# Optimization experiments

Measured on AMD Instinct MI355X. Metric: run time of the kernel, lower is better.

## Reference

```python
import jax, jax.numpy as jnp
import numpy as np

T, B, I, H = 512, 64, 512, 512

def setup_inputs() -> dict:
    key = jax.random.key(0)
    ks = jax.random.split(key, 7)
    s_in = 1.0 / np.sqrt(H)
    return {
        "input": jax.random.normal(ks[0], (T, B, I), dtype=jnp.float32),
        "h0": jax.random.normal(ks[1], (B, H), dtype=jnp.float32),
        "c0": jax.random.normal(ks[2], (B, H), dtype=jnp.float32),
        "W_ih": jax.random.uniform(ks[3], (4 * H, I), dtype=jnp.float32, minval=-s_in, maxval=s_in),
        "W_hh": jax.random.uniform(ks[4], (4 * H, H), dtype=jnp.float32, minval=-s_in, maxval=s_in),
        "b_ih": jax.random.uniform(ks[5], (4 * H,), dtype=jnp.float32, minval=-s_in, maxval=s_in),
        "b_hh": jax.random.uniform(ks[6], (4 * H,), dtype=jnp.float32, minval=-s_in, maxval=s_in),
    }

def reference(input, h0, c0, W_ih, W_hh, b_ih, b_hh):
    # Precompute input projections for all timesteps: [T, B, 4H]
    x_proj = jnp.einsum('tbi,gi->tbg', input, W_ih) + b_ih + b_hh

    def step(state, xp):
        h, c = state
        gates = xp + h @ W_hh.T  # [B, 4H]
        i_g, f_g, g_g, o_g = jnp.split(gates, 4, axis=-1)
        i_g = jax.nn.sigmoid(i_g)
        f_g = jax.nn.sigmoid(f_g)
        g_g = jnp.tanh(g_g)
        o_g = jax.nn.sigmoid(o_g)
        c_new = f_g * c + i_g * g_g
        h_new = o_g * jnp.tanh(c_new)
        return (h_new, c_new), h_new

    # reverse=True: process last timestep first, outputs placed at original indices
    (h_f, c_f), outputs = jax.lax.scan(step, (h0, c0), x_proj, reverse=True)
    return outputs, h_f, c_f
```

## Files before the change

### kernel.cpp

```cpp
#include <hip/hip_runtime.h>
#include <math.h>
#include <stdint.h>

#define T_ 512
#define B_ 64
#define I_ 512
#define H_ 512
#define G_ 2048
#define K_ 1024
#define NMR 32
#define NCOL 4
#define NBLK (NMR * NCOL)

typedef __bf16 bf16x8 __attribute__((ext_vector_type(8)));
typedef float f32x4 __attribute__((ext_vector_type(4)));
typedef int i32x4 __attribute__((ext_vector_type(4)));

#define OFF_W    ((size_t)0)
#define OFF_BIAS (OFF_W + (size_t)G_ * K_ * 2)
#define OFF_HSWZ (OFF_BIAS + (size_t)G_ * 4)
#define OFF_BAR  (OFF_HSWZ + (size_t)2 * H_ * B_ * 2)
#define OFF_XSWZ (OFF_BAR + 1024)


__global__ void prep_w(const float* __restrict__ W_ih, const float* __restrict__ W_hh,
                       const float* __restrict__ b_ih, const float* __restrict__ b_hh,
                       char* __restrict__ ws) {
    __bf16* W = (__bf16*)(ws + OFF_W);
    float* bias = (float*)(ws + OFF_BIAS);
    int idx = blockIdx.x * 256 + threadIdx.x;
    int g = idx >> 10;
    int k = idx & (K_ - 1);
    float v = (k < I_) ? W_ih[g * I_ + k] : W_hh[g * H_ + (k - I_)];
    W[idx] = (__bf16)v;
    if (idx < G_) bias[idx] = b_ih[idx] + b_hh[idx];
    if (idx < 256) ((unsigned*)(ws + OFF_BAR))[idx] = 0u;
}

__global__ void prep_x(const float* __restrict__ input, char* __restrict__ ws) {
    __bf16* xswz = (__bf16*)(ws + OFF_XSWZ);
    int s = blockIdx.x * 256 + threadIdx.x;
    int lane = s & 63;
    int nblk = (s >> 6) & 3;
    int kblk = (s >> 8) & 15;
    int t = s >> 12;
    int b = nblk * 16 + (lane & 15);
    int k = kblk * 32 + (lane >> 4) * 8;
    const float* src = input + ((size_t)t * B_ + b) * I_ + k;
    float4 v0 = *(const float4*)src;
    float4 v1 = *(const float4*)(src + 4);
    bf16x8 o;
    o[0]=(__bf16)v0.x; o[1]=(__bf16)v0.y; o[2]=(__bf16)v0.z; o[3]=(__bf16)v0.w;
    o[4]=(__bf16)v1.x; o[5]=(__bf16)v1.y; o[6]=(__bf16)v1.z; o[7]=(__bf16)v1.w;
    *(bf16x8*)(xswz + (size_t)s * 8) = o;
}

__global__ void prep_h0(const float* __restrict__ h0, char* __restrict__ ws) {
    __bf16* hswz0 = (__bf16*)(ws + OFF_HSWZ);
    int s = blockIdx.x * 256 + threadIdx.x;
    int lane = s & 63;
    int nblk = (s >> 6) & 3;
    int hk = s >> 8;
    int b = nblk * 16 + (lane & 15);
    int u = hk * 32 + (lane >> 4) * 8;
    const float* src = h0 + (size_t)b * H_ + u;
    float4 v0 = *(const float4*)src;
    float4 v1 = *(const float4*)(src + 4);
    bf16x8 o;
    o[0]=(__bf16)v0.x; o[1]=(__bf16)v0.y; o[2]=(__bf16)v0.z; o[3]=(__bf16)v0.w;
    o[4]=(__bf16)v1.x; o[5]=(__bf16)v1.y; o[6]=(__bf16)v1.z; o[7]=(__bf16)v1.w;
    *(bf16x8*)(hswz0 + (size_t)s * 8) = o;
}

__device__ __forceinline__ float sigmoid_f(float x) { return 1.f / (1.f + __expf(-x)); }
__device__ __forceinline__ float tanh_f(float x) { return 1.f - 2.f / (1.f + __expf(2.f * x)); }

__launch_bounds__(256, 1)
__global__ void lstm_persist(const float* __restrict__ c0, float* out,
                             char* __restrict__ ws) {
    __shared__ __bf16 xbuf[8192];
    __shared__ __bf16 hbuf[8192];
    __shared__ float gl[4][16][17];
    __shared__ __bf16 hstage[2][16][8];

    const __bf16* W = (const __bf16*)(ws + OFF_W);
    const float* bias = (const float*)(ws + OFF_BIAS);
    __bf16* Hswz = (__bf16*)(ws + OFF_HSWZ);
    const __bf16* Xswz = (const __bf16*)(ws + OFF_XSWZ);
    unsigned* flags = (unsigned*)(ws + OFF_BAR);

    const int tid = threadIdx.x;
    const int wave = tid >> 6;
    const int lane = tid & 63;
    const int l16 = lane & 15;
    const int quad = lane >> 4;
    const int wgM = blockIdx.x & 31;
    const int wgN = blockIdx.x >> 5;

    bf16x8 A[32];
    {
        const size_t arow = (size_t)(wave * H_ + wgM * 16 + l16) * K_ + quad * 8;
        #pragma unroll
        for (int ks = 0; ks < 32; ++ks)
            A[ks] = *(const bf16x8*)(W + arow + ks * 32);
    }

    const int cu_u = tid & 15;
    const int cu_bl = tid >> 4;
    const int hu = wgM * 16 + cu_u;
    const int batch = wgN * 16 + cu_bl;
    float creg = c0[(size_t)batch * H_ + hu];
    const float bias_i = bias[hu];
    const float bias_f = bias[H_ + hu];
    const float bias_g = bias[2 * H_ + hu];
    const float bias_o = bias[3 * H_ + hu];

    #define ISSUE_X(tt) do {                                                          \
        const __bf16* xb_ = Xswz + (size_t)(tt) * 32768;                              \
        _Pragma("unroll")                                                             \
        for (int i_ = 0; i_ < 4; ++i_) {                                              \
            const int kb_ = wave * 4 + i_;                                            \
            __builtin_amdgcn_global_load_lds(                                         \
                (const __attribute__((address_space(1))) void*)(xb_ + (size_t)((kb_ * 4 + wgN) * 64 + lane) * 8), \
                (__attribute__((address_space(3))) void*)(xbuf + kb_ * 512),          \
                16, 0, 0);                                                            \
        }                                                                             \
    } while (0)

    ISSUE_X(T_ - 1);
    asm volatile("s_waitcnt vmcnt(0)" ::: "memory");
    __builtin_amdgcn_sched_barrier(0);

    for (int t = T_ - 1; ; --t) {
        if (t < T_ - 1 && wave == 1) {
            const unsigned target = (unsigned)(T_ - 1 - t);
            const unsigned long long faddr =
                (unsigned long long)(uintptr_t)(flags + wgN * 64 + (lane & 31));
            unsigned cur;
            do {
                asm volatile("global_load_dword %0, %1, off sc0 sc1\n\t"
                             "s_waitcnt vmcnt(0)"
                             : "=v"(cur) : "v"(faddr) : "memory");
            } while (!__all(lane >= 32 || lane == wgM || cur >= target));
        }
        __builtin_amdgcn_sched_barrier(0);
        __builtin_amdgcn_s_barrier();
        __builtin_amdgcn_sched_barrier(0);

        {
            const __bf16* hb = Hswz + (size_t)((t + 1) & 1) * 32768;
            #pragma unroll
            for (int i = 0; i < 4; ++i) {
                const int hk = wave * 4 + i;
                __builtin_amdgcn_global_load_lds(
                    (const __attribute__((address_space(1))) void*)(hb + (size_t)((hk * 4 + wgN) * 64 + lane) * 8),
                    (__attribute__((address_space(3))) void*)(hbuf + hk * 512),
                    16, 0, 0x11);
            }
        }

        f32x4 ac0 = {0,0,0,0}, ac1 = {0,0,0,0}, ac2 = {0,0,0,0}, ac3 = {0,0,0,0};
        #pragma unroll
        for (int f = 0; f < 4; ++f) {
            bf16x8 b0 = *(const bf16x8*)(xbuf + (4*f+0) * 512 + lane * 8);
            bf16x8 b1 = *(const bf16x8*)(xbuf + (4*f+1) * 512 + lane * 8);
            bf16x8 b2 = *(const bf16x8*)(xbuf + (4*f+2) * 512 + lane * 8);
            bf16x8 b3 = *(const bf16x8*)(xbuf + (4*f+3) * 512 + lane * 8);
            ac0 = __builtin_amdgcn_mfma_f32_16x16x32_bf16(A[4*f+0], b0, ac0, 0, 0, 0);
            ac1 = __builtin_amdgcn_mfma_f32_16x16x32_bf16(A[4*f+1], b1, ac1, 0, 0, 0);
            ac2 = __builtin_amdgcn_mfma_f32_16x16x32_bf16(A[4*f+2], b2, ac2, 0, 0, 0);
            ac3 = __builtin_amdgcn_mfma_f32_16x16x32_bf16(A[4*f+3], b3, ac3, 0, 0, 0);
        }

        asm volatile("s_waitcnt vmcnt(0)" ::: "memory");
        __builtin_amdgcn_sched_barrier(0);
        __builtin_amdgcn_s_barrier();
        __builtin_amdgcn_sched_barrier(0);

        #pragma unroll
        for (int f = 0; f < 4; ++f) {
            bf16x8 b0 = *(const bf16x8*)(hbuf + (4*f+0) * 512 + lane * 8);
            bf16x8 b1 = *(const bf16x8*)(hbuf + (4*f+1) * 512 + lane * 8);
            bf16x8 b2 = *(const bf16x8*)(hbuf + (4*f+2) * 512 + lane * 8);
            bf16x8 b3 = *(const bf16x8*)(hbuf + (4*f+3) * 512 + lane * 8);
            ac0 = __builtin_amdgcn_mfma_f32_16x16x32_bf16(A[16+4*f+0], b0, ac0, 0, 0, 0);
            ac1 = __builtin_amdgcn_mfma_f32_16x16x32_bf16(A[16+4*f+1], b1, ac1, 0, 0, 0);
            ac2 = __builtin_amdgcn_mfma_f32_16x16x32_bf16(A[16+4*f+2], b2, ac2, 0, 0, 0);
            ac3 = __builtin_amdgcn_mfma_f32_16x16x32_bf16(A[16+4*f+3], b3, ac3, 0, 0, 0);
        }
        f32x4 accT = (ac0 + ac1) + (ac2 + ac3);

        #pragma unroll
        for (int r = 0; r < 4; ++r)
            gl[wave][quad * 4 + r][l16] = accT[r];
        __syncthreads();

        float ig = sigmoid_f(gl[0][cu_u][cu_bl] + bias_i);
        float fg = sigmoid_f(gl[1][cu_u][cu_bl] + bias_f);
        float gg = tanh_f(gl[2][cu_u][cu_bl] + bias_g);
        float og = sigmoid_f(gl[3][cu_u][cu_bl] + bias_o);
        float cn = fg * creg + ig * gg;
        creg = cn;
        float hn = og * tanh_f(cn);
        hstage[cu_u >> 3][cu_bl][cu_u & 7] = (__bf16)hn;
        __syncthreads();

        out[(size_t)t * B_ * H_ + (size_t)batch * H_ + hu] = hn;
        if (t == 0) {
            out[(size_t)T_ * B_ * H_ + (size_t)batch * H_ + hu] = hn;
            out[(size_t)T_ * B_ * H_ + B_ * H_ + (size_t)batch * H_ + hu] = cn;
            break;
        }
        ISSUE_X(t - 1);
        if (tid < 32) {
            i32x4 v = *(i32x4*)((__bf16*)hstage + tid * 8);
            const int lqc = tid >> 4, l16c = tid & 15;
            const int hk = wgM >> 1, q0 = (wgM & 1) * 2;
            size_t off = (size_t)((hk * 4 + wgN) * 64 + (q0 + lqc) * 16 + l16c) * 8;
            __bf16* dst = Hswz + (size_t)(t & 1) * 32768 + off;
            asm volatile("global_store_dwordx4 %0, %1, off sc0 sc1"
                         :: "v"(dst), "v"(v) : "memory");
        }
        asm volatile("s_waitcnt vmcnt(0)" ::: "memory");
        if (tid == 0) {
            const unsigned val = (unsigned)(T_ - t);
            const unsigned long long faddr =
                (unsigned long long)(uintptr_t)(flags + wgN * 64 + wgM);
            asm volatile("global_store_dword %0, %1, off sc0 sc1"
                         :: "v"(faddr), "v"(val) : "memory");
        }
    }
    #undef ISSUE_X
}

extern "C" void kernel_launch(void* const* d_in, const int* in_sizes, int n_in,
                              void* d_out, int out_size, void* d_ws, size_t ws_size,
                              hipStream_t stream) {
    const float* input = (const float*)d_in[0];
    const float* h0   = (const float*)d_in[1];
    const float* c0   = (const float*)d_in[2];
    const float* W_ih = (const float*)d_in[3];
    const float* W_hh = (const float*)d_in[4];
    const float* b_ih = (const float*)d_in[5];
    const float* b_hh = (const float*)d_in[6];
    float* out = (float*)d_out;
    char* ws = (char*)d_ws;

    prep_w<<<(G_ * K_) / 256, 256, 0, stream>>>(W_ih, W_hh, b_ih, b_hh, ws);
    prep_x<<<(T_ * I_ * B_ / 8) / 256, 256, 0, stream>>>(input, ws);
    prep_h0<<<16, 256, 0, stream>>>(h0, ws);
    lstm_persist<<<NBLK, 256, 0, stream>>>(c0, out, ws);
}
```

Baseline: 1.674 ms.

## Specialize waves for h publish and x prefetch, defer output store off critical path

Wave 0 alone now stores the new hidden-state slice and sets the flag, while waves 2-3 prefetch the next timestep's input slice. Previously all waves issued x loads and then waited on vmcnt before the flag store, so the flag publish was delayed by those loads. The per-step output store is deferred into the next iteration after the barrier, so it no longer precedes the flag publish. Empty asm constraints pin the weight registers to stop rematerialization, at some risk to register allocation.

```diff
diff --git a/kernel.cpp b/kernel.cpp
--- a/kernel.cpp
+++ b/kernel.cpp
@@ -104,6 +104,8 @@
         for (int ks = 0; ks < 32; ++ks)
             A[ks] = *(const bf16x8*)(W + arow + ks * 32);
     }
+    #pragma unroll
+    for (int ks = 0; ks < 32; ++ks) asm volatile("" : "+v"(A[ks]));
 
     const int cu_u = tid & 15;
     const int cu_bl = tid >> 4;
@@ -114,20 +116,19 @@
     const float bias_f = bias[H_ + hu];
     const float bias_g = bias[2 * H_ + hu];
     const float bias_o = bias[3 * H_ + hu];
-
-    #define ISSUE_X(tt) do {                                                          \
-        const __bf16* xb_ = Xswz + (size_t)(tt) * 32768;                              \
-        _Pragma("unroll")                                                             \
-        for (int i_ = 0; i_ < 4; ++i_) {                                              \
-            const int kb_ = wave * 4 + i_;                                            \
-            __builtin_amdgcn_global_load_lds(                                         \
-                (const __attribute__((address_space(1))) void*)(xb_ + (size_t)((kb_ * 4 + wgN) * 64 + lane) * 8), \
-                (__attribute__((address_space(3))) void*)(xbuf + kb_ * 512),          \
-                16, 0, 0);                                                            \
-        }                                                                             \
-    } while (0)
-
-    ISSUE_X(T_ - 1);
+    float hn = 0.f;
+
+    if (wave >= 2) {
+        const __bf16* xb = Xswz + (size_t)(T_ - 1) * 32768;
+        #pragma unroll
+        for (int i = 0; i < 8; ++i) {
+            const int kb = (wave - 2) * 8 + i;
+            __builtin_amdgcn_global_load_lds(
+                (const __attribute__((address_space(1))) void*)(xb + (size_t)((kb * 4 + wgN) * 64 + lane) * 8),
+                (__attribute__((address_space(3))) void*)(xbuf + kb * 512),
+                16, 0, 0);
+        }
+    }
     asm volatile("s_waitcnt vmcnt(0)" ::: "memory");
     __builtin_amdgcn_sched_barrier(0);
 
@@ -147,6 +148,12 @@
         __builtin_amdgcn_s_barrier();
         __builtin_amdgcn_sched_barrier(0);
 
+        #pragma unroll
+        for (int ks = 0; ks < 32; ++ks) asm volatile("" : "+v"(A[ks]));
+
+        if (t != T_ - 1)
+            out[(size_t)(t + 1) * B_ * H_ + (size_t)batch * H_ + hu] = hn;
+
         {
             const __bf16* hb = Hswz + (size_t)((t + 1) & 1) * 32768;
             #pragma unroll
@@ -201,36 +208,48 @@
         float og = sigmoid_f(gl[3][cu_u][cu_bl] + bias_o);
         float cn = fg * creg + ig * gg;
         creg = cn;
-        float hn = og * tanh_f(cn);
+        hn = og * tanh_f(cn);
         hstage[cu_u >> 3][cu_bl][cu_u & 7] = (__bf16)hn;
         __syncthreads();
 
-        out[(size_t)t * B_ * H_ + (size_t)batch * H_ + hu] = hn;
         if (t == 0) {
+            out[(size_t)batch * H_ + hu] = hn;
             out[(size_t)T_ * B_ * H_ + (size_t)batch * H_ + hu] = hn;
             out[(size_t)T_ * B_ * H_ + B_ * H_ + (size_t)batch * H_ + hu] = cn;
             break;
         }
-        ISSUE_X(t - 1);
-        if (tid < 32) {
-            i32x4 v = *(i32x4*)((__bf16*)hstage + tid * 8);
-            const int lqc = tid >> 4, l16c = tid & 15;
-            const int hk = wgM >> 1, q0 = (wgM & 1) * 2;
-            size_t off = (size_t)((hk * 4 + wgN) * 64 + (q0 + lqc) * 16 + l16c) * 8;
-            __bf16* dst = Hswz + (size_t)(t & 1) * 32768 + off;
-            asm volatile("global_store_dwordx4 %0, %1, off sc0 sc1"
-                         :: "v"(dst), "v"(v) : "memory");
-        }
-        asm volatile("s_waitcnt vmcnt(0)" ::: "memory");
-        if (tid == 0) {
-            const unsigned val = (unsigned)(T_ - t);
-            const unsigned long long faddr =
-                (unsigned long long)(uintptr_t)(flags + wgN * 64 + wgM);
-            asm volatile("global_store_dword %0, %1, off sc0 sc1"
-                         :: "v"(faddr), "v"(val) : "memory");
+
+        if (wave == 0) {
+            if (lane < 32) {
+                i32x4 v = *(i32x4*)((__bf16*)hstage + lane * 8);
+                const int lqc = lane >> 4, l16c = lane & 15;
+                const int hk = wgM >> 1, q0 = (wgM & 1) * 2;
+                size_t off = (size_t)((hk * 4 + wgN) * 64 + (q0 + lqc) * 16 + l16c) * 8;
+                __bf16* dst = Hswz + (size_t)(t & 1) * 32768 + off;
+                asm volatile("global_store_dwordx4 %0, %1, off sc0 sc1"
+                             :: "v"(dst), "v"(v) : "memory");
+            }
+            asm volatile("s_waitcnt vmcnt(0)" ::: "memory");
+            if (lane == 0) {
+                const unsigned val = (unsigned)(T_ - t);
+                const unsigned long long faddr =
+                    (unsigned long long)(uintptr_t)(flags + wgN * 64 + wgM);
+                asm volatile("global_store_dword %0, %1, off sc0 sc1"
+                             :: "v"(faddr), "v"(val) : "memory");
+            }
+        } else if (wave >= 2) {
+            const __bf16* xb = Xswz + (size_t)(t - 1) * 32768;
+            #pragma unroll
+            for (int i = 0; i < 8; ++i) {
+                const int kb = (wave - 2) * 8 + i;
+                __builtin_amdgcn_global_load_lds(
+                    (const __attribute__((address_space(1))) void*)(xb + (size_t)((kb * 4 + wgN) * 64 + lane) * 8),
+                    (__attribute__((address_space(3))) void*)(xbuf + kb * 512),
+                    16, 0, 0);
+            }
+            asm volatile("s_waitcnt vmcnt(0)" ::: "memory");
         }
     }
-    #undef ISSUE_X
 }
 
 extern "C" void kernel_launch(void* const* d_in, const int* in_sizes, int n_in,
```

Result: faster. 1.566 ms (-6.5%).
